# Performance work log

Measured on AMD Instinct MI355X. Metric: run time of the kernel, lower is better.

The kernel has to match this reference:

```python
import jax, jax.numpy as jnp
import numpy as np

D_MODEL = 4096
N_HEADS = 32
N_KV_HEADS = 8
HEAD_DIM = D_MODEL // N_HEADS  # 128
SEQ = 2048
BATCH = 1
ROPE_BASE = 10000.0


def build_rope_cache(max_seq_len, head_dim, base=10000.0):
    half = head_dim // 2
    pos = jnp.arange(max_seq_len, dtype=jnp.float32)
    inv_freqs = 1.0 / (base ** (jnp.arange(half, dtype=jnp.float32) / half))
    angles = pos[:, None] * inv_freqs[None, :]  # (S, half)
    return jnp.cos(angles), jnp.sin(angles)


def apply_rope(t, cos, sin):
    # t: (B, H, S, D); cos/sin: (S, D//2) broadcast over batch & heads.
    t_even = t[..., 0::2]
    t_odd = t[..., 1::2]
    c = cos[None, None, :, :]
    s = sin[None, None, :, :]
    rot_even = t_even * c - t_odd * s
    rot_odd = t_even * s + t_odd * c
    # interleave back into even/odd slots
    return jnp.stack([rot_even, rot_odd], axis=-1).reshape(t.shape)


def setup_inputs() -> dict:
    key = jax.random.key(0)
    kx, kq, kk, kv, ko = jax.random.split(key, 5)
    bound = 1.0 / np.sqrt(D_MODEL)
    x = jax.random.normal(kx, (BATCH, SEQ, D_MODEL), dtype=jnp.float32)
    # torch Linear weights: (out_features, in_features)
    wq = jax.random.uniform(kq, (N_HEADS * HEAD_DIM, D_MODEL), minval=-bound, maxval=bound, dtype=jnp.float32)
    wk = jax.random.uniform(kk, (N_KV_HEADS * HEAD_DIM, D_MODEL), minval=-bound, maxval=bound, dtype=jnp.float32)
    wv = jax.random.uniform(kv, (N_KV_HEADS * HEAD_DIM, D_MODEL), minval=-bound, maxval=bound, dtype=jnp.float32)
    wo = jax.random.uniform(ko, (D_MODEL, D_MODEL), minval=-bound, maxval=bound, dtype=jnp.float32)
    attn_mask = jnp.tril(jnp.ones((SEQ, SEQ), dtype=jnp.int32))[None, None, :, :]
    return {"x": x, "wq": wq, "wk": wk, "wv": wv, "wo": wo, "attn_mask": attn_mask}


def reference(x, wq, wk, wv, wo, attn_mask):
    B, S, _ = x.shape
    cos, sin = build_rope_cache(SEQ, HEAD_DIM, ROPE_BASE)
    cos, sin = cos[:S], sin[:S]
    q = (x @ wq.T).reshape(B, S, N_HEADS, HEAD_DIM).transpose(0, 2, 1, 3)      # (B,H,S,D)
    k = (x @ wk.T).reshape(B, S, N_KV_HEADS, HEAD_DIM).transpose(0, 2, 1, 3)   # (B,Hkv,S,D)
    v = (x @ wv.T).reshape(B, S, N_KV_HEADS, HEAD_DIM).transpose(0, 2, 1, 3)
    q = apply_rope(q, cos, sin)
    k = apply_rope(k, cos, sin)
    n_rep = N_HEADS // N_KV_HEADS
    if n_rep > 1:
        k = jnp.repeat(k, n_rep, axis=1)
        v = jnp.repeat(v, n_rep, axis=1)
    scores = jnp.einsum('bhqd,bhkd->bhqk', q, k) / jnp.sqrt(jnp.float32(HEAD_DIM))
    scores = jnp.where(attn_mask == 0, -jnp.inf, scores)
    attn = jax.nn.softmax(scores, axis=-1)
    out = jnp.einsum('bhqk,bhkd->bhqd', attn, v)
    out = out.transpose(0, 2, 1, 3).reshape(B, S, D_MODEL)
    return out @ wo.T
```

## Files before the change

kernel.cpp:

```cpp
#include <hip/hip_runtime.h>
#include <hip/hip_bf16.h>

typedef float f32x4 __attribute__((ext_vector_type(4)));
typedef __bf16 bf16x8 __attribute__((ext_vector_type(8)));

__device__ __forceinline__ void gld_lds16(const void* g, void* l) {
  __builtin_amdgcn_global_load_lds((const __attribute__((address_space(1))) void*)g,
                                   (__attribute__((address_space(3))) void*)l, 16, 0, 0);
}

__global__ void cvt_f32_bf16(const float* __restrict__ in, __bf16* __restrict__ out,
                             int n8) {
  int idx = blockIdx.x * blockDim.x + threadIdx.x;
  if (idx >= n8) return;
  f32x4 a = *(const f32x4*)(in + (size_t)idx * 8);
  f32x4 b = *(const f32x4*)(in + (size_t)idx * 8 + 4);
  bf16x8 o;
#pragma unroll
  for (int j = 0; j < 4; ++j) { o[j] = (__bf16)a[j]; o[4 + j] = (__bf16)b[j]; }
  *(bf16x8*)(out + (size_t)idx * 8) = o;
}

__global__ void build_trig(float* __restrict__ trig) {
  int idx = blockIdx.x * blockDim.x + threadIdx.x;
  if (idx >= 2048 * 64) return;
  int i = idx & 63, s = idx >> 6;
  float ang = (float)s * powf(10000.0f, -(float)i * (1.0f / 64.0f));
  float sn, cs;
  sincosf(ang, &sn, &cs);
  trig[idx * 2] = cs;
  trig[idx * 2 + 1] = sn;
}

__global__ void rope_bf16(__bf16* __restrict__ T, const float* __restrict__ trig,
                          int stride, int nh_mask, int nh_shift, float mul, int total) {
  int idx = blockIdx.x * blockDim.x + threadIdx.x;
  if (idx >= total) return;
  int i = idx & 63;
  int h = (idx >> 6) & nh_mask;
  int s = idx >> (6 + nh_shift);
  float cs = trig[(s * 64 + i) * 2];
  float sn = trig[(s * 64 + i) * 2 + 1];
  __bf16* p = T + (size_t)s * stride + h * 128 + 2 * i;
  float e = (float)p[0], o = (float)p[1];
  p[0] = (__bf16)((e * cs - o * sn) * mul);
  p[1] = (__bf16)((e * sn + o * cs) * mul);
}

__global__ __launch_bounds__(256) void transpose_v(const __bf16* __restrict__ KVb,
                                                   __bf16* __restrict__ Vt) {
  __shared__ __bf16 T[64][72];
  const int tid = threadIdx.x;
  const int s0 = blockIdx.x * 64, d0 = blockIdx.y * 64;
  const int r = tid >> 3, c8 = (tid & 7) * 8;
#pragma unroll
  for (int i = 0; i < 2; ++i) {
    int row = i * 32 + r;
    *(bf16x8*)&T[row][c8] = *(const bf16x8*)&KVb[(size_t)(s0 + row) * 2048 + 1024 + d0 + c8];
  }
  __syncthreads();
#pragma unroll
  for (int i = 0; i < 2; ++i) {
    int drow = i * 32 + r;
    bf16x8 o;
#pragma unroll
    for (int j = 0; j < 8; ++j) o[j] = T[c8 + j][drow];
    *(bf16x8*)&Vt[(size_t)(d0 + drow) * 2048 + s0 + c8] = o;
  }
}

template <int BM, int BN, typename OutT>
__global__ __launch_bounds__(256) void gemm_bf16(const __bf16* __restrict__ A,
                                                 const __bf16* __restrict__ B0,
                                                 const __bf16* __restrict__ B1,
                                                 int Nsplit, OutT* __restrict__ C,
                                                 int M, int N, int K) {
  constexpr int MI = BM / 32, NJ = BN / 32;
  constexpr int RA = BM / 32, RB = BN / 32;
  __shared__ __bf16 As[BM * 64] __attribute__((aligned(16)));
  __shared__ __bf16 Bs[BN * 64] __attribute__((aligned(16)));

  const int tid = threadIdx.x;
  const int lane = tid & 63;
  const int w = tid >> 6;
  const int nwg = gridDim.x * gridDim.y;
  const int orig = blockIdx.y * gridDim.x + blockIdx.x;
  const int wgid = (orig & 7) * (nwg >> 3) + (orig >> 3);
  const int m0 = (wgid % gridDim.x) * BM;
  const int n0 = (wgid / gridDim.x) * BN;
  const int li = lane & 15, lg = lane >> 4;

  const __bf16* bsrc[RB];
#pragma unroll
  for (int i = 0; i < RB; ++i) {
    int slot = i * 256 + w * 64 + lane;
    int row = slot >> 3;
    int sch = (slot & 7) ^ (row & 7);
    int n = n0 + row;
    bsrc[i] = (n < Nsplit ? B0 + (size_t)n * K : B1 + (size_t)(n - Nsplit) * K) +
              sch * 8;
  }
  const __bf16* asrc[RA];
#pragma unroll
  for (int i = 0; i < RA; ++i) {
    int slot = i * 256 + w * 64 + lane;
    int row = slot >> 3;
    int sch = (slot & 7) ^ (row & 7);
    asrc[i] = A + (size_t)(m0 + row) * K + sch * 8;
  }

  const int wr = (w >> 1) * (BM / 2);
  const int wc = (w & 1) * (BN / 2);

  f32x4 acc[MI][NJ] = {};

  for (int k0 = 0; k0 < K; k0 += 64) {
    __syncthreads();
#pragma unroll
    for (int i = 0; i < RA; ++i)
      gld_lds16(asrc[i] + k0, &As[(i * 256 + w * 64) * 8]);
#pragma unroll
    for (int i = 0; i < RB; ++i)
      gld_lds16(bsrc[i] + k0, &Bs[(i * 256 + w * 64) * 8]);
    __syncthreads();

#pragma unroll
    for (int u = 0; u < 2; ++u) {
      bf16x8 af[MI], bfr[NJ];
#pragma unroll
      for (int mi = 0; mi < MI; ++mi)
        af[mi] = *(const bf16x8*)&As[(wr + mi * 16 + li) * 64 +
                                     (((u * 4 + lg) ^ (li & 7)) * 8)];
#pragma unroll
      for (int nj = 0; nj < NJ; ++nj)
        bfr[nj] = *(const bf16x8*)&Bs[(wc + nj * 16 + li) * 64 +
                                      (((u * 4 + lg) ^ (li & 7)) * 8)];
#pragma unroll
      for (int mi = 0; mi < MI; ++mi)
#pragma unroll
        for (int nj = 0; nj < NJ; ++nj)
          acc[mi][nj] = __builtin_amdgcn_mfma_f32_16x16x32_bf16(af[mi], bfr[nj],
                                                                acc[mi][nj], 0, 0, 0);
    }
  }

  const int crow = lg * 4;
#pragma unroll
  for (int mi = 0; mi < MI; ++mi)
#pragma unroll
    for (int nj = 0; nj < NJ; ++nj)
#pragma unroll
      for (int r = 0; r < 4; ++r)
        C[(size_t)(m0 + wr + mi * 16 + crow + r) * N + (n0 + wc + nj * 16 + li)] =
            (OutT)acc[mi][nj][r];
}

__global__ __launch_bounds__(256) void attn_fwd_v4(const __bf16* __restrict__ Q,
                                                   const __bf16* __restrict__ KVb,
                                                   const __bf16* __restrict__ Vt,
                                                   __bf16* __restrict__ O) {
  const int tid = threadIdx.x;
  const int lane = tid & 63;
  const int w = tid >> 6;
  const int orig = blockIdx.x;
  const int chunk = orig & 7;
  const int wkk = orig >> 3;
  const int h = chunk * 4 + (wkk & 3);
  const int pair = wkk >> 2;
  const int kvh = h >> 2;

  __shared__ __bf16 Ks[2][64 * 128] __attribute__((aligned(16)));
  __shared__ __bf16 Vts[128 * 64] __attribute__((aligned(16)));
  __shared__ __bf16 Ps[4][16 * 72] __attribute__((aligned(16)));

  const int li = lane & 15, lg = lane >> 4;

  auto stage_k = [&](int k0, int buf) {
#pragma unroll
    for (int i = 0; i < 4; ++i) {
      int slot = i * 256 + tid;
      int row = slot >> 4;
      int sch = (slot & 15) ^ (row & 7);
      gld_lds16(&KVb[(size_t)(k0 + row) * 2048 + kvh * 128 + sch * 8],
                &Ks[buf][(i * 256 + w * 64) * 8]);
    }
  };
  auto stage_v = [&](int k0) {
#pragma unroll
    for (int i = 0; i < 4; ++i) {
      int slot = i * 256 + tid;
      int row = slot >> 3;
      int sch = (slot & 7) ^ (row & 7);
      gld_lds16(&Vt[(size_t)(kvh * 128 + row) * 2048 + k0 + sch * 8],
                &Vts[(i * 256 + w * 64) * 8]);
    }
  };

#pragma unroll 1
  for (int pass = 0; pass < 2; ++pass) {
    const int m0 = ((pass == 0) ? (15 - pair) : pair) * 128;
    const int rbase = m0 + w * 32;

    bf16x8 qf[2][4];
#pragma unroll
    for (int mt = 0; mt < 2; ++mt) {
      const __bf16* qrow = Q + (size_t)(rbase + mt * 16 + li) * 4096 + h * 128;
#pragma unroll
      for (int kc = 0; kc < 4; ++kc) qf[mt][kc] = *(const bf16x8*)(qrow + kc * 32 + lg * 8);
    }

    f32x4 accO[2][8] = {};
    float plane[2][4] = {};

    const int wmax = rbase + 31;
    const int ntile = (m0 + 128) >> 6;

    stage_k(0, 0);
    __syncthreads();

    for (int t = 0; t < ntile; ++t) {
      const int k0 = t * 64;
      const int cur = t & 1;
      stage_v(k0);
      if (t + 1 < ntile) stage_k(k0 + 64, cur ^ 1);

      const bool active = (k0 <= wmax);
      bf16x8 pa[2][2];
      if (active) {
        f32x4 s[2][4] = {};
#pragma unroll
        for (int nt = 0; nt < 4; ++nt)
#pragma unroll
          for (int kc = 0; kc < 4; ++kc) {
            bf16x8 kf = *(const bf16x8*)&Ks[cur][(li + 16 * nt) * 128 +
                                                (((4 * kc + lg) ^ (li & 7)) * 8)];
            s[0][nt] = __builtin_amdgcn_mfma_f32_16x16x32_bf16(qf[0][kc], kf, s[0][nt], 0, 0, 0);
            s[1][nt] = __builtin_amdgcn_mfma_f32_16x16x32_bf16(qf[1][kc], kf, s[1][nt], 0, 0, 0);
          }

#pragma unroll
        for (int mt = 0; mt < 2; ++mt) {
          const int qb = rbase + mt * 16;
          const bool needmask = (k0 + 63 > qb);
#pragma unroll
          for (int r = 0; r < 4; ++r) {
            const int qa = qb + lg * 4 + r;
            float v0 = s[mt][0][r], v1 = s[mt][1][r];
            float v2 = s[mt][2][r], v3 = s[mt][3][r];
            if (needmask) {
              if (k0 + 0 + li > qa) v0 = -INFINITY;
              if (k0 + 16 + li > qa) v1 = -INFINITY;
              if (k0 + 32 + li > qa) v2 = -INFINITY;
              if (k0 + 48 + li > qa) v3 = -INFINITY;
            }
            float p0 = exp2f(v0), p1 = exp2f(v1);
            float p2 = exp2f(v2), p3 = exp2f(v3);
            plane[mt][r] += (p0 + p1) + (p2 + p3);
            int qrow = lg * 4 + r;
            Ps[w][qrow * 72 + li]      = (__bf16)p0;
            Ps[w][qrow * 72 + li + 16] = (__bf16)p1;
            Ps[w][qrow * 72 + li + 32] = (__bf16)p2;
            Ps[w][qrow * 72 + li + 48] = (__bf16)p3;
          }
          pa[mt][0] = *(const bf16x8*)&Ps[w][li * 72 + lg * 8];
          pa[mt][1] = *(const bf16x8*)&Ps[w][li * 72 + 32 + lg * 8];
        }
      }

      __syncthreads();

      if (active) {
#pragma unroll
        for (int dt = 0; dt < 8; ++dt)
#pragma unroll
          for (int kc = 0; kc < 2; ++kc) {
            bf16x8 vf = *(const bf16x8*)&Vts[(li + 16 * dt) * 64 +
                                             (((4 * kc + lg) ^ (li & 7)) * 8)];
            accO[0][dt] = __builtin_amdgcn_mfma_f32_16x16x32_bf16(pa[0][kc], vf, accO[0][dt], 0, 0, 0);
            accO[1][dt] = __builtin_amdgcn_mfma_f32_16x16x32_bf16(pa[1][kc], vf, accO[1][dt], 0, 0, 0);
          }
      }

      __syncthreads();
    }

#pragma unroll
    for (int mt = 0; mt < 2; ++mt) {
      float inv[4];
#pragma unroll
      for (int r = 0; r < 4; ++r) {
        float sum = plane[mt][r];
        sum += __shfl_xor(sum, 1);
        sum += __shfl_xor(sum, 2);
        sum += __shfl_xor(sum, 4);
        sum += __shfl_xor(sum, 8);
        inv[r] = 1.0f / sum;
      }
#pragma unroll
      for (int dt = 0; dt < 8; ++dt)
#pragma unroll
        for (int r = 0; r < 4; ++r)
          O[(size_t)(rbase + mt * 16 + lg * 4 + r) * 4096 + h * 128 + dt * 16 + li] =
              (__bf16)(accO[mt][dt][r] * inv[r]);
    }
  }
}

extern "C" void kernel_launch(void* const* d_in, const int* in_sizes, int n_in,
                              void* d_out, int out_size, void* d_ws, size_t ws_size,
                              hipStream_t stream) {
  const float* x  = (const float*)d_in[0];
  const float* wq = (const float*)d_in[1];
  const float* wk = (const float*)d_in[2];
  const float* wv = (const float*)d_in[3];
  const float* wo = (const float*)d_in[4];
  float* out = (float*)d_out;

  const int S = 2048, D = 4096;
  char* ws = (char*)d_ws;
  __bf16* xb  = (__bf16*)ws;
  __bf16* Qb  = (__bf16*)(ws + 16777216);
  __bf16* KVb = (__bf16*)(ws + 33554432);
  __bf16* Vt  = (__bf16*)(ws + 41943040);
  __bf16* wb  = (__bf16*)(ws + 46137344);
  float*  trig = (float*)(ws + 79691776);
  __bf16* AOb = xb;

  const float qscale = 0.08838834764831845f * 1.4426950408889634f;

  cvt_f32_bf16<<<(S * D / 8 + 255) / 256, 256, 0, stream>>>(x, xb, S * D / 8);
  cvt_f32_bf16<<<(D * D / 8 + 255) / 256, 256, 0, stream>>>(wq, wb, D * D / 8);
  gemm_bf16<128, 128, __bf16><<<dim3(16, 32), 256, 0, stream>>>(
      xb, wb, wb, 1 << 30, Qb, S, D, D);

  cvt_f32_bf16<<<(1024 * D / 8 + 255) / 256, 256, 0, stream>>>(wk, wb, 1024 * D / 8);
  cvt_f32_bf16<<<(1024 * D / 8 + 255) / 256, 256, 0, stream>>>(wv, wb + (size_t)1024 * D,
                                                               1024 * D / 8);
  gemm_bf16<64, 128, __bf16><<<dim3(32, 16), 256, 0, stream>>>(
      xb, wb, wb + (size_t)1024 * D, 1024, KVb, S, 2048, D);

  build_trig<<<(2048 * 64 + 255) / 256, 256, 0, stream>>>(trig);
  rope_bf16<<<(S * 32 * 64 + 255) / 256, 256, 0, stream>>>(Qb, trig, 4096, 31, 5,
                                                           qscale, S * 32 * 64);
  rope_bf16<<<(S * 8 * 64 + 255) / 256, 256, 0, stream>>>(KVb, trig, 2048, 7, 3,
                                                          1.0f, S * 8 * 64);
  transpose_v<<<dim3(32, 16), 256, 0, stream>>>(KVb, Vt);

  attn_fwd_v4<<<256, 256, 0, stream>>>(Qb, KVb, Vt, AOb);

  cvt_f32_bf16<<<(D * D / 8 + 255) / 256, 256, 0, stream>>>(wo, wb, D * D / 8);
  gemm_bf16<128, 128, float><<<dim3(16, 32), 256, 0, stream>>>(
      AOb, wb, wb, 1 << 30, out, S, D, D);
}
```

Measured before the change: 375.2 us.

## Pipeline attention loads with partial waitcnt barriers and transposed score MFMA layout

Replaces the full __syncthreads in the attention loop with raw s_barrier plus partial vmcnt waits, so the next K tile and the V tile stay in flight while scores are computed. The score MFMA operands are swapped so each lane holds four consecutive keys for one query. This allows packed 4-wide P stores to LDS and a per-lane row sum reduced with fewer shuffles. It also raises wave priority around the MFMA blocks and always issues a K stage, which may be a dummy reload, to keep the vmcnt counts fixed. The hand-counted waitcnt values risk races if the load counts differ from what is assumed.

Result: no change. 376.4 us (+0.3%).

```diff
diff --git a/kernel.cpp b/kernel.cpp
--- a/kernel.cpp
+++ b/kernel.cpp
@@ -2,6 +2,7 @@
 #include <hip/hip_bf16.h>
 
 typedef float f32x4 __attribute__((ext_vector_type(4)));
+typedef __bf16 bf16x4 __attribute__((ext_vector_type(4)));
 typedef __bf16 bf16x8 __attribute__((ext_vector_type(8)));
 
 __device__ __forceinline__ void gld_lds16(const void* g, void* l) {
@@ -155,7 +156,7 @@
             (OutT)acc[mi][nj][r];
 }
 
-__global__ __launch_bounds__(256) void attn_fwd_v4(const __bf16* __restrict__ Q,
+__global__ __launch_bounds__(256) void attn_fwd_v5(const __bf16* __restrict__ Q,
                                                    const __bf16* __restrict__ KVb,
                                                    const __bf16* __restrict__ Vt,
                                                    __bf16* __restrict__ O) {
@@ -171,7 +172,7 @@
 
   __shared__ __bf16 Ks[2][64 * 128] __attribute__((aligned(16)));
   __shared__ __bf16 Vts[128 * 64] __attribute__((aligned(16)));
-  __shared__ __bf16 Ps[4][16 * 72] __attribute__((aligned(16)));
+  __shared__ __bf16 Ps[4][32 * 72] __attribute__((aligned(16)));
 
   const int li = lane & 15, lg = lane >> 4;
 
@@ -210,66 +211,72 @@
     }
 
     f32x4 accO[2][8] = {};
-    float plane[2][4] = {};
+    float plane[2] = {0.f, 0.f};
 
     const int wmax = rbase + 31;
     const int ntile = (m0 + 128) >> 6;
 
     stage_k(0, 0);
-    __syncthreads();
-
+
+#pragma unroll 1
     for (int t = 0; t < ntile; ++t) {
       const int k0 = t * 64;
       const int cur = t & 1;
       stage_v(k0);
-      if (t + 1 < ntile) stage_k(k0 + 64, cur ^ 1);
+      stage_k(t + 1 < ntile ? k0 + 64 : 0, cur ^ 1);
+
+      asm volatile("s_waitcnt vmcnt(8)" ::: "memory");
+      __builtin_amdgcn_s_barrier();
+      __builtin_amdgcn_sched_barrier(0);
+      asm volatile("" ::: "memory");
 
       const bool active = (k0 <= wmax);
       bf16x8 pa[2][2];
       if (active) {
-        f32x4 s[2][4] = {};
+        f32x4 s2[4][2] = {};
+        __builtin_amdgcn_s_setprio(1);
 #pragma unroll
         for (int nt = 0; nt < 4; ++nt)
 #pragma unroll
           for (int kc = 0; kc < 4; ++kc) {
             bf16x8 kf = *(const bf16x8*)&Ks[cur][(li + 16 * nt) * 128 +
                                                 (((4 * kc + lg) ^ (li & 7)) * 8)];
-            s[0][nt] = __builtin_amdgcn_mfma_f32_16x16x32_bf16(qf[0][kc], kf, s[0][nt], 0, 0, 0);
-            s[1][nt] = __builtin_amdgcn_mfma_f32_16x16x32_bf16(qf[1][kc], kf, s[1][nt], 0, 0, 0);
+            s2[nt][0] = __builtin_amdgcn_mfma_f32_16x16x32_bf16(kf, qf[0][kc], s2[nt][0], 0, 0, 0);
+            s2[nt][1] = __builtin_amdgcn_mfma_f32_16x16x32_bf16(kf, qf[1][kc], s2[nt][1], 0, 0, 0);
           }
+        __builtin_amdgcn_s_setprio(0);
 
 #pragma unroll
         for (int mt = 0; mt < 2; ++mt) {
           const int qb = rbase + mt * 16;
+          const int q = qb + li;
           const bool needmask = (k0 + 63 > qb);
 #pragma unroll
-          for (int r = 0; r < 4; ++r) {
-            const int qa = qb + lg * 4 + r;
-            float v0 = s[mt][0][r], v1 = s[mt][1][r];
-            float v2 = s[mt][2][r], v3 = s[mt][3][r];
-            if (needmask) {
-              if (k0 + 0 + li > qa) v0 = -INFINITY;
-              if (k0 + 16 + li > qa) v1 = -INFINITY;
-              if (k0 + 32 + li > qa) v2 = -INFINITY;
-              if (k0 + 48 + li > qa) v3 = -INFINITY;
+          for (int nt = 0; nt < 4; ++nt) {
+            bf16x4 pk;
+#pragma unroll
+            for (int r = 0; r < 4; ++r) {
+              const int key = k0 + 16 * nt + lg * 4 + r;
+              float v = s2[nt][mt][r];
+              if (needmask && key > q) v = -INFINITY;
+              float p = exp2f(v);
+              plane[mt] += p;
+              pk[r] = (__bf16)p;
             }
-            float p0 = exp2f(v0), p1 = exp2f(v1);
-            float p2 = exp2f(v2), p3 = exp2f(v3);
-            plane[mt][r] += (p0 + p1) + (p2 + p3);
-            int qrow = lg * 4 + r;
-            Ps[w][qrow * 72 + li]      = (__bf16)p0;
-            Ps[w][qrow * 72 + li + 16] = (__bf16)p1;
-            Ps[w][qrow * 72 + li + 32] = (__bf16)p2;
-            Ps[w][qrow * 72 + li + 48] = (__bf16)p3;
+            *(bf16x4*)&Ps[w][(mt * 16 + li) * 72 + 16 * nt + lg * 4] = pk;
           }
-          pa[mt][0] = *(const bf16x8*)&Ps[w][li * 72 + lg * 8];
-          pa[mt][1] = *(const bf16x8*)&Ps[w][li * 72 + 32 + lg * 8];
+          pa[mt][0] = *(const bf16x8*)&Ps[w][(mt * 16 + li) * 72 + lg * 8];
+          pa[mt][1] = *(const bf16x8*)&Ps[w][(mt * 16 + li) * 72 + 32 + lg * 8];
         }
       }
 
-      __syncthreads();
+      asm volatile("s_waitcnt vmcnt(4)" ::: "memory");
+      __builtin_amdgcn_s_barrier();
+      __builtin_amdgcn_sched_barrier(0);
+      asm volatile("" ::: "memory");
 
       if (active) {
+        __builtin_amdgcn_s_setprio(1);
 #pragma unroll
         for (int dt = 0; dt < 8; ++dt)
 #pragma unroll
@@ -279,23 +286,22 @@
             accO[0][dt] = __builtin_amdgcn_mfma_f32_16x16x32_bf16(pa[0][kc], vf, accO[0][dt], 0, 0, 0);
             accO[1][dt] = __builtin_amdgcn_mfma_f32_16x16x32_bf16(pa[1][kc], vf, accO[1][dt], 0, 0, 0);
           }
+        __builtin_amdgcn_s_setprio(0);
       }
 
-      __syncthreads();
+      __builtin_amdgcn_s_barrier();
+      __builtin_amdgcn_sched_barrier(0);
+      asm volatile("" ::: "memory");
     }
 
 #pragma unroll
     for (int mt = 0; mt < 2; ++mt) {
+      float sum = plane[mt];
+      sum += __shfl_xor(sum, 16);
+      sum += __shfl_xor(sum, 32);
       float inv[4];
 #pragma unroll
-      for (int r = 0; r < 4; ++r) {
-        float sum = plane[mt][r];
-        sum += __shfl_xor(sum, 1);
-        sum += __shfl_xor(sum, 2);
-        sum += __shfl_xor(sum, 4);
-        sum += __shfl_xor(sum, 8);
-        inv[r] = 1.0f / sum;
-      }
+      for (int r = 0; r < 4; ++r) inv[r] = 1.0f / __shfl(sum, lg * 4 + r);
 #pragma unroll
       for (int dt = 0; dt < 8; ++dt)
 #pragma unroll
@@ -346,7 +352,7 @@
                                                           1.0f, S * 8 * 64);
   transpose_v<<<dim3(32, 16), 256, 0, stream>>>(KVb, Vt);
 
-  attn_fwd_v4<<<256, 256, 0, stream>>>(Qb, KVb, Vt, AOb);
+  attn_fwd_v5<<<256, 256, 0, stream>>>(Qb, KVb, Vt, AOb);
 
   cvt_f32_bf16<<<(D * D / 8 + 255) / 256, 256, 0, stream>>>(wo, wb, D * D / 8);
   gemm_bf16<128, 128, float><<<dim3(16, 32), 256, 0, stream>>>(
```
